# Performance work log

Hardware: AMD Instinct MI355X
Metric: run time of the kernel (lower is better)

Reference implementation:

```python
import jax, jax.numpy as jnp
import numpy as np

NEG_INF = -1e30

def setup_inputs() -> dict:
    key = jax.random.key(0)
    kC, kQ, kw = jax.random.split(key, 3)
    B, D, Lc, Lq = 32, 128, 2048, 64
    C = jax.random.normal(kC, (B, D, Lc), dtype=jnp.float32)
    Q = jax.random.normal(kQ, (B, D, Lq), dtype=jnp.float32)
    qmask = jnp.ones((B, Lq), dtype=jnp.float32)
    # trilinear weight, uniform(-sqrt(1/D), sqrt(1/D)) as in the torch init
    lim = (1.0 / D) ** 0.5
    w = jax.random.uniform(kw, (3 * D,), dtype=jnp.float32, minval=-lim, maxval=lim)
    return {"C": C, "Q": Q, "qmask": qmask, "w": w}

def reference(C, Q, qmask, w):
    # C: (B, D, Lc), Q: (B, D, Lq), qmask: (B, Lq), w: (3D,)
    Ct = jnp.transpose(C, (0, 2, 1))  # (B, Lc, D)
    Qt = jnp.transpose(Q, (0, 2, 1))  # (B, Lq, D)
    D = Ct.shape[-1]
    w1, w2, w3 = w[:D], w[D:2 * D], w[2 * D:]
    # trilinear similarity S[b,i,j] = Ct[b,i].w1 + Qt[b,j].w2 + (Ct[b,i]*Qt[b,j]).w3
    # computed WITHOUT the (B,Lc,Lq,3D) intermediate
    sc = Ct @ w1                                   # (B, Lc)
    sq = Qt @ w2                                   # (B, Lq)
    scq = jnp.einsum('bid,bjd->bij', Ct * w3, Qt)  # (B, Lc, Lq)
    S = sc[:, :, None] + sq[None if False else slice(None), None, :] + scq  # (B, Lc, Lq)
    m = qmask[:, None, :]                          # (B, 1, Lq)
    S1 = jax.nn.softmax(S * m + (1.0 - m) * NEG_INF, axis=2)  # over query axis
    S2 = jax.nn.softmax(S, axis=1)                             # over context axis
    A = jnp.einsum('bij,bjd->bid', S1, Qt)                     # (B, Lc, D)
    S1S2T = jnp.einsum('bij,bkj->bik', S1, S2)                 # (B, Lc, Lc) via S1 @ S2^T
    Bm = jnp.einsum('bik,bkd->bid', S1S2T, Ct)                 # (B, Lc, D)
    out = jnp.concatenate([Ct, A, Ct * A, Ct * Bm], axis=2)    # (B, Lc, 4D)
    # dropout is identity in eval mode
    return jnp.transpose(out, (0, 2, 1))                       # (B, 4D, Lc)
```

## Files before the change

kernel.cpp:

```cpp
#include <hip/hip_runtime.h>

#define LC 2048
#define DD 128
#define LQ 64
#define NPART 16
#define PAD 136

typedef unsigned short u16;
typedef unsigned int u32;
typedef __attribute__((ext_vector_type(8))) short bf16x8;
typedef __attribute__((ext_vector_type(4))) float f32x4;

__device__ inline u16 f2b(float f) {
  u32 u = __float_as_uint(f);
  u32 r = (u + 0x7fffu + ((u >> 16) & 1u)) >> 16;
  return (u16)r;
}
__device__ inline float b2f(u16 u) { return __uint_as_float(((u32)u) << 16); }
__device__ inline u32 pack2(float a, float b) {
  return (u32)f2b(a) | ((u32)f2b(b) << 16);
}

__global__ __launch_bounds__(256) void k13(const float* __restrict__ C,
                                           const float* __restrict__ Q,
                                           const float* __restrict__ w,
                                           const float* __restrict__ qmask,
                                           u16* __restrict__ S1g,
                                           float* __restrict__ Tu_part,
                                           float* __restrict__ Z_part, int B) {
  __shared__ u16 ldsA[128 * PAD];
  __shared__ u16 ldsB[64 * PAD];
  __shared__ float scL[128];
  __shared__ float sqs[64];
  __shared__ float mkS[64];
  int b = blockIdx.y, bx = blockIdx.x;
  int i0 = bx * 128, t = threadIdx.x;
  const float* Cb = C + (size_t)b * DD * LC;
  const float* Qb = Q + (size_t)b * DD * LQ;
  if (t < 64) mkS[t] = qmask[b * LQ + t];
  int i_st = t & 127, dh = t >> 7;
  float scp = 0.f;
  {
    const float* Cp = Cb + (size_t)dh * 64 * LC + i0 + i_st;
#pragma unroll
    for (int dp = 0; dp < 32; ++dp) {
      int d = dh * 64 + 2 * dp;
      float c0 = Cp[(size_t)(2 * dp) * LC];
      float c1 = Cp[(size_t)(2 * dp + 1) * LC];
      scp = fmaf(c0, w[d], fmaf(c1, w[d + 1], scp));
      *(u32*)&ldsA[i_st * PAD + d] = pack2(c0, c1);
    }
    if (dh == 0) scL[i_st] = scp;
  }
  {
    int j = t & 63, dg = t >> 6;
    const float* Qp = Qb + j;
    float sqp = 0.f;
#pragma unroll
    for (int dp = 0; dp < 16; ++dp) {
      int d = dg * 32 + 2 * dp;
      float q0 = Qp[(size_t)d * LQ];
      float q1 = Qp[(size_t)(d + 1) * LQ];
      sqp = fmaf(q0, w[DD + d], fmaf(q1, w[DD + d + 1], sqp));
      *(u32*)&ldsB[j * PAD + d] = pack2(q0 * w[2 * DD + d], q1 * w[2 * DD + d + 1]);
    }
    ((float*)&ldsB[j * PAD + 128])[dg] = sqp;
  }
  __syncthreads();
  if (dh == 1) scL[i_st] += scp;
  if (t < 64) {
    const float* pp = (const float*)&ldsB[t * PAD + 128];
    sqs[t] = pp[0] + pp[1] + pp[2] + pp[3];
  }
  int lane = t & 63, wv = t >> 6;
  int lr = lane & 15, kg = lane >> 4;
  f32x4 acc[2][4];
#pragma unroll
  for (int mt = 0; mt < 2; ++mt)
#pragma unroll
    for (int nt = 0; nt < 4; ++nt) acc[mt][nt] = (f32x4){0.f, 0.f, 0.f, 0.f};
#pragma unroll
  for (int ks = 0; ks < 4; ++ks) {
    bf16x8 af[2], bf[4];
#pragma unroll
    for (int mt = 0; mt < 2; ++mt)
      af[mt] = *(bf16x8*)&ldsA[((wv * 2 + mt) * 16 + lr) * PAD + ks * 32 + kg * 8];
#pragma unroll
    for (int nt = 0; nt < 4; ++nt)
      bf[nt] = *(bf16x8*)&ldsB[(nt * 16 + lr) * PAD + ks * 32 + kg * 8];
#pragma unroll
    for (int mt = 0; mt < 2; ++mt)
#pragma unroll
      for (int nt = 0; nt < 4; ++nt)
        acc[mt][nt] = __builtin_amdgcn_mfma_f32_16x16x32_bf16(af[mt], bf[nt],
                                                              acc[mt][nt], 0, 0, 0);
  }
  __syncthreads();
#pragma unroll
  for (int mt = 0; mt < 2; ++mt) {
    int ib = (wv * 2 + mt) * 16 + kg * 4;
    float ev[4][4];
    float ps[4] = {0.f, 0.f, 0.f, 0.f};
#pragma unroll
    for (int nt = 0; nt < 4; ++nt) {
      int j = nt * 16 + lr;
      float sqv = sqs[j];
      float mkv = mkS[j];
#pragma unroll
      for (int r = 0; r < 4; ++r) {
        float e = __expf(acc[mt][nt][r] + scL[ib + r] + sqv);
        ev[nt][r] = e;
        ps[r] = fmaf(mkv, e, ps[r]);
      }
    }
#pragma unroll
    for (int r = 0; r < 4; ++r) {
      ps[r] += __shfl_xor(ps[r], 1, 64);
      ps[r] += __shfl_xor(ps[r], 2, 64);
      ps[r] += __shfl_xor(ps[r], 4, 64);
      ps[r] += __shfl_xor(ps[r], 8, 64);
    }
#pragma unroll
    for (int nt = 0; nt < 4; ++nt) {
      int j = nt * 16 + lr;
      u32 pk[2] = {pack2(ev[nt][0], ev[nt][1]), pack2(ev[nt][2], ev[nt][3])};
      *(uint2*)&ldsB[j * PAD + ib] = *(uint2*)pk;
    }
    if (lr == 0) {
#pragma unroll
      for (int r = 0; r < 4; ++r) {
        int i = ib + r;
        ((float*)&ldsB[(i & 63) * PAD + 128])[i >> 6] = 1.f / fmaxf(ps[r], 1e-30f);
      }
    }
  }
  {
    int d = t >> 1, half = t & 1;
    const float* src = Cb + (size_t)d * LC + i0 + half * 64;
#pragma unroll
    for (int ip = 0; ip < 16; ++ip) {
      float4 v = *(const float4*)&src[ip * 4];
      u32 pk[2] = {pack2(v.x, v.y), pack2(v.z, v.w)};
      *(uint2*)&ldsA[d * PAD + half * 64 + ip * 4] = *(uint2*)pk;
    }
  }
  __syncthreads();
  if (t < 64) {
    const u32* row = (const u32*)&ldsB[t * PAD];
    float z = 0.f;
#pragma unroll
    for (int q = 0; q < 64; ++q) {
      u32 v = row[q];
      z += b2f((u16)v) + b2f((u16)(v >> 16));
    }
    Z_part[((size_t)bx * B + b) * LQ + t] = z;
  }
  {
    int i = t >> 1, half = t & 1;
    float inv = ((float*)&ldsB[(i & 63) * PAD + 128])[i >> 6];
    u32 opk[16];
#pragma unroll
    for (int q = 0; q < 16; ++q) {
      int j = half * 32 + 2 * q;
      float a0 = b2f(ldsB[j * PAD + i]) * mkS[j] * inv;
      float a1 = b2f(ldsB[(j + 1) * PAD + i]) * mkS[j + 1] * inv;
      opk[q] = pack2(a0, a1);
    }
    u16* dst = S1g + ((size_t)b * LC + i0 + i) * LQ + half * 32;
#pragma unroll
    for (int q = 0; q < 4; ++q) *(uint4*)&dst[q * 8] = *(uint4*)&opk[q * 4];
  }
  f32x4 tacc[2][4];
#pragma unroll
  for (int mt = 0; mt < 2; ++mt)
#pragma unroll
    for (int nt = 0; nt < 4; ++nt) tacc[mt][nt] = (f32x4){0.f, 0.f, 0.f, 0.f};
#pragma unroll
  for (int ks = 0; ks < 4; ++ks) {
    bf16x8 af[2], bf[4];
#pragma unroll
    for (int mt = 0; mt < 2; ++mt)
      af[mt] = *(bf16x8*)&ldsA[((wv * 2 + mt) * 16 + lr) * PAD + ks * 32 + kg * 8];
#pragma unroll
    for (int nt = 0; nt < 4; ++nt)
      bf[nt] = *(bf16x8*)&ldsB[(nt * 16 + lr) * PAD + ks * 32 + kg * 8];
#pragma unroll
    for (int mt = 0; mt < 2; ++mt)
#pragma unroll
      for (int nt = 0; nt < 4; ++nt)
        tacc[mt][nt] = __builtin_amdgcn_mfma_f32_16x16x32_bf16(af[mt], bf[nt],
                                                               tacc[mt][nt], 0, 0, 0);
  }
  float* Tp = Tu_part + ((size_t)bx * B + b) * LQ * DD;
#pragma unroll
  for (int mt = 0; mt < 2; ++mt)
#pragma unroll
    for (int nt = 0; nt < 4; ++nt) {
      int j = nt * 16 + lr;
      int db = (wv * 2 + mt) * 16 + kg * 4;
      *(f32x4*)&Tp[(size_t)j * DD + db] = tacc[mt][nt];
    }
}

__global__ __launch_bounds__(256) void k3b(const float* __restrict__ Tu_part,
                                           const float* __restrict__ Z_part,
                                           u16* __restrict__ TzT, int B) {
  __shared__ float Tsm[16][68];
  __shared__ float ziL[64];
  int b = blockIdx.y, d0 = blockIdx.x * 16;
  int t = threadIdx.x;
  int dd = t & 15, jg = t >> 4;
  float acc[4] = {};
#pragma unroll
  for (int p = 0; p < NPART; ++p) {
    const float* src = Tu_part + ((size_t)p * B + b) * LQ * DD + d0 + dd;
#pragma unroll
    for (int jj = 0; jj < 4; ++jj) acc[jj] += src[(jg * 4 + jj) * DD];
  }
  if (t < 64) {
    float z = 0.f;
#pragma unroll
    for (int p = 0; p < NPART; ++p) z += Z_part[((size_t)p * B + b) * LQ + t];
    ziL[t] = 1.f / z;
  }
  *(float4*)&Tsm[dd][jg * 4] = make_float4(acc[0], acc[1], acc[2], acc[3]);
  __syncthreads();
  if (t < 128) {
    int d = t >> 3, seg = t & 7;
    u32 pk[4];
#pragma unroll
    for (int q = 0; q < 4; ++q) {
      int j = seg * 8 + q * 2;
      pk[q] = pack2(Tsm[d][j] * ziL[j], Tsm[d][j + 1] * ziL[j + 1]);
    }
    *(uint4*)&TzT[((size_t)b * DD + d0 + d) * LQ + seg * 8] = *(uint4*)pk;
  }
}

__global__ __launch_bounds__(256) void k4(const u16* __restrict__ S1g,
                                          const float* __restrict__ Q,
                                          const u16* __restrict__ TzT,
                                          const float* __restrict__ C,
                                          float* __restrict__ out) {
  int b = blockIdx.y, i0 = blockIdx.x * 128, t = threadIdx.x;
  int lane = t & 63, wv = t >> 6;
  int lr = lane & 15, kg = lane >> 4;
  bf16x8 Bf[2][2];
#pragma unroll
  for (int it = 0; it < 2; ++it) {
    size_t ri = (size_t)b * LC + i0 + wv * 32 + it * 16 + lr;
#pragma unroll
    for (int ks = 0; ks < 2; ++ks)
      Bf[it][ks] = *(const bf16x8*)&S1g[ri * LQ + ks * 32 + kg * 8];
  }
  const float* Qb = Q + (size_t)b * DD * LQ;
  const u16* Tzb = TzT + (size_t)b * DD * LQ;
  const float* Cb = C + (size_t)b * DD * LC + i0;
  float* outb = out + (size_t)b * 4 * DD * LC + i0;
#pragma unroll
  for (int dt = 0; dt < 8; ++dt) {
    int da = dt * 16 + lr;
    bf16x8 QA[2], TA[2];
#pragma unroll
    for (int ks = 0; ks < 2; ++ks) {
      const float* qp = Qb + da * LQ + ks * 32 + kg * 8;
      float4 q0 = *(const float4*)qp;
      float4 q1 = *(const float4*)(qp + 4);
      u32 pk[4] = {pack2(q0.x, q0.y), pack2(q0.z, q0.w), pack2(q1.x, q1.y),
                   pack2(q1.z, q1.w)};
      QA[ks] = *(bf16x8*)pk;
      TA[ks] = *(const bf16x8*)&Tzb[da * LQ + ks * 32 + kg * 8];
    }
#pragma unroll
    for (int it = 0; it < 2; ++it) {
      f32x4 accA = {0.f, 0.f, 0.f, 0.f}, accB = {0.f, 0.f, 0.f, 0.f};
      accA = __builtin_amdgcn_mfma_f32_16x16x32_bf16(QA[0], Bf[it][0], accA, 0, 0, 0);
      accA = __builtin_amdgcn_mfma_f32_16x16x32_bf16(QA[1], Bf[it][1], accA, 0, 0, 0);
      accB = __builtin_amdgcn_mfma_f32_16x16x32_bf16(TA[0], Bf[it][0], accB, 0, 0, 0);
      accB = __builtin_amdgcn_mfma_f32_16x16x32_bf16(TA[1], Bf[it][1], accB, 0, 0, 0);
      int ii = wv * 32 + it * 16 + lr;
#pragma unroll
      for (int r = 0; r < 4; ++r) {
        int d = dt * 16 + kg * 4 + r;
        float c = Cb[(size_t)d * LC + ii];
        float a = accA[r], bm = accB[r];
        outb[(size_t)d * LC + ii] = c;
        outb[(size_t)(DD + d) * LC + ii] = a;
        outb[(size_t)(2 * DD + d) * LC + ii] = c * a;
        outb[(size_t)(3 * DD + d) * LC + ii] = c * bm;
      }
    }
  }
}

extern "C" void kernel_launch(void* const* d_in, const int* in_sizes, int n_in,
                              void* d_out, int out_size, void* d_ws, size_t ws_size,
                              hipStream_t stream) {
  const float* C = (const float*)d_in[0];
  const float* Q = (const float*)d_in[1];
  const float* qmask = (const float*)d_in[2];
  const float* w = (const float*)d_in[3];
  float* out = (float*)d_out;
  int B = in_sizes[2] / LQ;

  char* p = (char*)d_ws;
  u16* S1g = (u16*)p;           p += (size_t)B * LC * LQ * 2;
  u16* TzT = (u16*)p;           p += (size_t)B * DD * LQ * 2;
  float* Tu_part = (float*)p;   p += (size_t)NPART * B * LQ * DD * 4;
  float* Z_part = (float*)p;

  k13<<<dim3(NPART, B), 256, 0, stream>>>(C, Q, w, qmask, S1g, Tu_part, Z_part, B);
  k3b<<<dim3(DD / 16, B), 256, 0, stream>>>(Tu_part, Z_part, TzT, B);
  k4<<<dim3(LC / 128, B), 256, 0, stream>>>(S1g, Q, TzT, C, out);
}
```

Measured before the change: 71.58 us.

## Halve row tiles, pre-convert Q to bf16, vectorize k4 output stores

The context tile in k13 and k4 shrinks from 128 to 64 rows. This doubles the grid and the number of partial sums, with LDS buffers and reductions reorganized to match. k3b now also converts Q to bf16 once, so k4 no longer repacks Q in every block. k4 swaps its MFMA operand roles so each lane holds 4 consecutive context positions, which lets it read C and write all four output planes with float4 accesses. The trade-off is that k3b must now reduce twice as many Tu partials, and the grid gets more blocks with less work each.

```diff
diff --git a/kernel.cpp b/kernel.cpp
--- a/kernel.cpp
+++ b/kernel.cpp
@@ -3,8 +3,9 @@
 #define LC 2048
 #define DD 128
 #define LQ 64
-#define NPART 16
-#define PAD 136
+#define NPART 32
+#define PADA 136
+#define PADC 72
 
 typedef unsigned short u16;
 typedef unsigned int u32;
@@ -28,29 +29,28 @@
                                            u16* __restrict__ S1g,
                                            float* __restrict__ Tu_part,
                                            float* __restrict__ Z_part, int B) {
-  __shared__ u16 ldsA[128 * PAD];
-  __shared__ u16 ldsB[64 * PAD];
-  __shared__ float scL[128];
-  __shared__ float sqs[64];
-  __shared__ float mkS[64];
+  __shared__ u16 ldsA[128 * PADC];
+  __shared__ u16 ldsB[64 * PADA];
+  __shared__ float scp4[4][64], sqp4[4][64];
+  __shared__ float scL[64], sqs[64], mkS[64], invL[64];
   int b = blockIdx.y, bx = blockIdx.x;
-  int i0 = bx * 128, t = threadIdx.x;
+  int i0 = bx * 64, t = threadIdx.x;
   const float* Cb = C + (size_t)b * DD * LC;
   const float* Qb = Q + (size_t)b * DD * LQ;
   if (t < 64) mkS[t] = qmask[b * LQ + t];
-  int i_st = t & 127, dh = t >> 7;
-  float scp = 0.f;
-  {
-    const float* Cp = Cb + (size_t)dh * 64 * LC + i0 + i_st;
-#pragma unroll
-    for (int dp = 0; dp < 32; ++dp) {
-      int d = dh * 64 + 2 * dp;
-      float c0 = Cp[(size_t)(2 * dp) * LC];
-      float c1 = Cp[(size_t)(2 * dp + 1) * LC];
+  {
+    int i = t & 63, dg = t >> 6;
+    const float* Cp = Cb + i0 + i;
+    float scp = 0.f;
+#pragma unroll
+    for (int dp = 0; dp < 16; ++dp) {
+      int d = dg * 32 + 2 * dp;
+      float c0 = Cp[(size_t)d * LC];
+      float c1 = Cp[(size_t)(d + 1) * LC];
       scp = fmaf(c0, w[d], fmaf(c1, w[d + 1], scp));
-      *(u32*)&ldsA[i_st * PAD + d] = pack2(c0, c1);
-    }
-    if (dh == 0) scL[i_st] = scp;
+      *(u32*)&ldsA[i * PADA + d] = pack2(c0, c1);
+    }
+    scp4[dg][i] = scp;
   }
   {
     int j = t & 63, dg = t >> 6;
@@ -62,53 +62,44 @@
       float q0 = Qp[(size_t)d * LQ];
       float q1 = Qp[(size_t)(d + 1) * LQ];
       sqp = fmaf(q0, w[DD + d], fmaf(q1, w[DD + d + 1], sqp));
-      *(u32*)&ldsB[j * PAD + d] = pack2(q0 * w[2 * DD + d], q1 * w[2 * DD + d + 1]);
-    }
-    ((float*)&ldsB[j * PAD + 128])[dg] = sqp;
+      *(u32*)&ldsB[j * PADA + d] = pack2(q0 * w[2 * DD + d], q1 * w[2 * DD + d + 1]);
+    }
+    sqp4[dg][j] = sqp;
   }
   __syncthreads();
-  if (dh == 1) scL[i_st] += scp;
-  if (t < 64) {
-    const float* pp = (const float*)&ldsB[t * PAD + 128];
-    sqs[t] = pp[0] + pp[1] + pp[2] + pp[3];
+  if (t < 64) scL[t] = scp4[0][t] + scp4[1][t] + scp4[2][t] + scp4[3][t];
+  else if (t < 128) {
+    int j = t - 64;
+    sqs[j] = sqp4[0][j] + sqp4[1][j] + sqp4[2][j] + sqp4[3][j];
   }
   int lane = t & 63, wv = t >> 6;
   int lr = lane & 15, kg = lane >> 4;
-  f32x4 acc[2][4];
-#pragma unroll
-  for (int mt = 0; mt < 2; ++mt)
-#pragma unroll
-    for (int nt = 0; nt < 4; ++nt) acc[mt][nt] = (f32x4){0.f, 0.f, 0.f, 0.f};
+  f32x4 acc[4];
+#pragma unroll
+  for (int nt = 0; nt < 4; ++nt) acc[nt] = (f32x4){0.f, 0.f, 0.f, 0.f};
 #pragma unroll
   for (int ks = 0; ks < 4; ++ks) {
-    bf16x8 af[2], bf[4];
-#pragma unroll
-    for (int mt = 0; mt < 2; ++mt)
-      af[mt] = *(bf16x8*)&ldsA[((wv * 2 + mt) * 16 + lr) * PAD + ks * 32 + kg * 8];
+    bf16x8 af = *(bf16x8*)&ldsA[(wv * 16 + lr) * PADA + ks * 32 + kg * 8];
+    bf16x8 bf[4];
 #pragma unroll
     for (int nt = 0; nt < 4; ++nt)
-      bf[nt] = *(bf16x8*)&ldsB[(nt * 16 + lr) * PAD + ks * 32 + kg * 8];
-#pragma unroll
-    for (int mt = 0; mt < 2; ++mt)
-#pragma unroll
-      for (int nt = 0; nt < 4; ++nt)
-        acc[mt][nt] = __builtin_amdgcn_mfma_f32_16x16x32_bf16(af[mt], bf[nt],
-                                                              acc[mt][nt], 0, 0, 0);
+      bf[nt] = *(bf16x8*)&ldsB[(nt * 16 + lr) * PADA + ks * 32 + kg * 8];
+#pragma unroll
+    for (int nt = 0; nt < 4; ++nt)
+      acc[nt] = __builtin_amdgcn_mfma_f32_16x16x32_bf16(af, bf[nt], acc[nt], 0, 0, 0);
   }
   __syncthreads();
-#pragma unroll
-  for (int mt = 0; mt < 2; ++mt) {
-    int ib = (wv * 2 + mt) * 16 + kg * 4;
+  {
+    int ib = wv * 16 + kg * 4;
     float ev[4][4];
     float ps[4] = {0.f, 0.f, 0.f, 0.f};
 #pragma unroll
     for (int nt = 0; nt < 4; ++nt) {
       int j = nt * 16 + lr;
-      float sqv = sqs[j];
-      float mkv = mkS[j];
+      float sqv = sqs[j], mkv = mkS[j];
 #pragma unroll
       for (int r = 0; r < 4; ++r) {
-        float e = __expf(acc[mt][nt][r] + scL[ib + r] + sqv);
+        float e = __expf(acc[nt][r] + scL[ib + r] + sqv);
         ev[nt][r] = e;
         ps[r] = fmaf(mkv, e, ps[r]);
       }
@@ -124,51 +115,48 @@
     for (int nt = 0; nt < 4; ++nt) {
       int j = nt * 16 + lr;
       u32 pk[2] = {pack2(ev[nt][0], ev[nt][1]), pack2(ev[nt][2], ev[nt][3])};
-      *(uint2*)&ldsB[j * PAD + ib] = *(uint2*)pk;
+      *(uint2*)&ldsB[j * PADC + ib] = *(uint2*)pk;
     }
     if (lr == 0) {
 #pragma unroll
-      for (int r = 0; r < 4; ++r) {
-        int i = ib + r;
-        ((float*)&ldsB[(i & 63) * PAD + 128])[i >> 6] = 1.f / fmaxf(ps[r], 1e-30f);
-      }
+      for (int r = 0; r < 4; ++r) invL[ib + r] = 1.f / fmaxf(ps[r], 1e-30f);
     }
   }
   {
     int d = t >> 1, half = t & 1;
-    const float* src = Cb + (size_t)d * LC + i0 + half * 64;
-#pragma unroll
-    for (int ip = 0; ip < 16; ++ip) {
+    const float* src = Cb + (size_t)d * LC + i0 + half * 32;
+#pragma unroll
+    for (int ip = 0; ip < 8; ++ip) {
       float4 v = *(const float4*)&src[ip * 4];
       u32 pk[2] = {pack2(v.x, v.y), pack2(v.z, v.w)};
-      *(uint2*)&ldsA[d * PAD + half * 64 + ip * 4] = *(uint2*)pk;
+      *(uint2*)&ldsA[d * PADC + half * 32 + ip * 4] = *(uint2*)pk;
     }
   }
   __syncthreads();
   if (t < 64) {
-    const u32* row = (const u32*)&ldsB[t * PAD];
+    const u32* row = (const u32*)&ldsB[t * PADC];
     float z = 0.f;
 #pragma unroll
-    for (int q = 0; q < 64; ++q) {
+    for (int q = 0; q < 32; ++q) {
       u32 v = row[q];
       z += b2f((u16)v) + b2f((u16)(v >> 16));
     }
     Z_part[((size_t)bx * B + b) * LQ + t] = z;
   }
   {
-    int i = t >> 1, half = t & 1;
-    float inv = ((float*)&ldsB[(i & 63) * PAD + 128])[i >> 6];
-    u32 opk[16];
-#pragma unroll
-    for (int q = 0; q < 16; ++q) {
-      int j = half * 32 + 2 * q;
-      float a0 = b2f(ldsB[j * PAD + i]) * mkS[j] * inv;
-      float a1 = b2f(ldsB[(j + 1) * PAD + i]) * mkS[j + 1] * inv;
+    int i = t >> 2, q4 = t & 3;
+    float inv = invL[i];
+    u32 opk[8];
+#pragma unroll
+    for (int q = 0; q < 8; ++q) {
+      int j = q4 * 16 + 2 * q;
+      float a0 = b2f(ldsB[j * PADC + i]) * mkS[j] * inv;
+      float a1 = b2f(ldsB[(j + 1) * PADC + i]) * mkS[j + 1] * inv;
       opk[q] = pack2(a0, a1);
     }
-    u16* dst = S1g + ((size_t)b * LC + i0 + i) * LQ + half * 32;
-#pragma unroll
-    for (int q = 0; q < 4; ++q) *(uint4*)&dst[q * 8] = *(uint4*)&opk[q * 4];
+    u16* dst = S1g + ((size_t)b * LC + i0 + i) * LQ + q4 * 16;
+    *(uint4*)&dst[0] = *(uint4*)&opk[0];
+    *(uint4*)&dst[8] = *(uint4*)&opk[4];
   }
   f32x4 tacc[2][4];
 #pragma unroll
@@ -176,14 +164,14 @@
 #pragma unroll
     for (int nt = 0; nt < 4; ++nt) tacc[mt][nt] = (f32x4){0.f, 0.f, 0.f, 0.f};
 #pragma unroll
-  for (int ks = 0; ks < 4; ++ks) {
+  for (int ks = 0; ks < 2; ++ks) {
     bf16x8 af[2], bf[4];
 #pragma unroll
     for (int mt = 0; mt < 2; ++mt)
-      af[mt] = *(bf16x8*)&ldsA[((wv * 2 + mt) * 16 + lr) * PAD + ks * 32 + kg * 8];
+      af[mt] = *(bf16x8*)&ldsA[((wv * 2 + mt) * 16 + lr) * PADC + ks * 32 + kg * 8];
 #pragma unroll
     for (int nt = 0; nt < 4; ++nt)
-      bf[nt] = *(bf16x8*)&ldsB[(nt * 16 + lr) * PAD + ks * 32 + kg * 8];
+      bf[nt] = *(bf16x8*)&ldsB[(nt * 16 + lr) * PADC + ks * 32 + kg * 8];
 #pragma unroll
     for (int mt = 0; mt < 2; ++mt)
 #pragma unroll
@@ -204,11 +192,19 @@
 
 __global__ __launch_bounds__(256) void k3b(const float* __restrict__ Tu_part,
                                            const float* __restrict__ Z_part,
-                                           u16* __restrict__ TzT, int B) {
+                                           const float* __restrict__ Q,
+                                           u16* __restrict__ TzT,
+                                           u16* __restrict__ Qbf, int B) {
   __shared__ float Tsm[16][68];
   __shared__ float ziL[64];
   int b = blockIdx.y, d0 = blockIdx.x * 16;
   int t = threadIdx.x;
+  {
+    int dq = d0 + (t >> 4), jq = (t & 15) * 4;
+    const float* qp = Q + ((size_t)b * DD + dq) * LQ + jq;
+    u32 pk[2] = {pack2(qp[0], qp[1]), pack2(qp[2], qp[3])};
+    *(uint2*)&Qbf[((size_t)b * DD + dq) * LQ + jq] = *(uint2*)pk;
+  }
   int dd = t & 15, jg = t >> 4;
   float acc[4] = {};
 #pragma unroll
@@ -238,58 +234,48 @@
 }
 
 __global__ __launch_bounds__(256) void k4(const u16* __restrict__ S1g,
-                                          const float* __restrict__ Q,
+                                          const u16* __restrict__ Qbf,
                                           const u16* __restrict__ TzT,
                                           const float* __restrict__ C,
                                           float* __restrict__ out) {
-  int b = blockIdx.y, i0 = blockIdx.x * 128, t = threadIdx.x;
+  int b = blockIdx.y, i0 = blockIdx.x * 64, t = threadIdx.x;
   int lane = t & 63, wv = t >> 6;
   int lr = lane & 15, kg = lane >> 4;
-  bf16x8 Bf[2][2];
-#pragma unroll
-  for (int it = 0; it < 2; ++it) {
-    size_t ri = (size_t)b * LC + i0 + wv * 32 + it * 16 + lr;
-#pragma unroll
-    for (int ks = 0; ks < 2; ++ks)
-      Bf[it][ks] = *(const bf16x8*)&S1g[ri * LQ + ks * 32 + kg * 8];
-  }
-  const float* Qb = Q + (size_t)b * DD * LQ;
+  bf16x8 Af[2];
+  {
+    size_t ri = ((size_t)b * LC + i0 + wv * 16 + lr) * LQ;
+    Af[0] = *(const bf16x8*)&S1g[ri + kg * 8];
+    Af[1] = *(const bf16x8*)&S1g[ri + 32 + kg * 8];
+  }
+  const u16* Qb = Qbf + (size_t)b * DD * LQ;
   const u16* Tzb = TzT + (size_t)b * DD * LQ;
   const float* Cb = C + (size_t)b * DD * LC + i0;
   float* outb = out + (size_t)b * 4 * DD * LC + i0;
-#pragma unroll
-  for (int dt = 0; dt < 8; ++dt) {
-    int da = dt * 16 + lr;
-    bf16x8 QA[2], TA[2];
+  int irow = wv * 16 + kg * 4;
+#pragma unroll
+  for (int nt = 0; nt < 8; ++nt) {
+    int d = nt * 16 + lr;
+    bf16x8 QB[2], TB[2];
 #pragma unroll
     for (int ks = 0; ks < 2; ++ks) {
-      const float* qp = Qb + da * LQ + ks * 32 + kg * 8;
-      float4 q0 = *(const float4*)qp;
-      float4 q1 = *(const float4*)(qp + 4);
-      u32 pk[4] = {pack2(q0.x, q0.y), pack2(q0.z, q0.w), pack2(q1.x, q1.y),
-                   pack2(q1.z, q1.w)};
-      QA[ks] = *(bf16x8*)pk;
-      TA[ks] = *(const bf16x8*)&Tzb[da * LQ + ks * 32 + kg * 8];
-    }
-#pragma unroll
-    for (int it = 0; it < 2; ++it) {
-      f32x4 accA = {0.f, 0.f, 0.f, 0.f}, accB = {0.f, 0.f, 0.f, 0.f};
-      accA = __builtin_amdgcn_mfma_f32_16x16x32_bf16(QA[0], Bf[it][0], accA, 0, 0, 0);
-      accA = __builtin_amdgcn_mfma_f32_16x16x32_bf16(QA[1], Bf[it][1], accA, 0, 0, 0);
-      accB = __builtin_amdgcn_mfma_f32_16x16x32_bf16(TA[0], Bf[it][0], accB, 0, 0, 0);
-      accB = __builtin_amdgcn_mfma_f32_16x16x32_bf16(TA[1], Bf[it][1], accB, 0, 0, 0);
-      int ii = wv * 32 + it * 16 + lr;
-#pragma unroll
-      for (int r = 0; r < 4; ++r) {
-        int d = dt * 16 + kg * 4 + r;
-        float c = Cb[(size_t)d * LC + ii];
-        float a = accA[r], bm = accB[r];
-        outb[(size_t)d * LC + ii] = c;
-        outb[(size_t)(DD + d) * LC + ii] = a;
-        outb[(size_t)(2 * DD + d) * LC + ii] = c * a;
-        outb[(size_t)(3 * DD + d) * LC + ii] = c * bm;
-      }
-    }
+      QB[ks] = *(const bf16x8*)&Qb[(size_t)d * LQ + ks * 32 + kg * 8];
+      TB[ks] = *(const bf16x8*)&Tzb[(size_t)d * LQ + ks * 32 + kg * 8];
+    }
+    f32x4 accA = {0.f, 0.f, 0.f, 0.f}, accB = {0.f, 0.f, 0.f, 0.f};
+    accA = __builtin_amdgcn_mfma_f32_16x16x32_bf16(Af[0], QB[0], accA, 0, 0, 0);
+    accA = __builtin_amdgcn_mfma_f32_16x16x32_bf16(Af[1], QB[1], accA, 0, 0, 0);
+    accB = __builtin_amdgcn_mfma_f32_16x16x32_bf16(Af[0], TB[0], accB, 0, 0, 0);
+    accB = __builtin_amdgcn_mfma_f32_16x16x32_bf16(Af[1], TB[1], accB, 0, 0, 0);
+    float4 c4 = *(const float4*)&Cb[(size_t)d * LC + irow];
+    float4 oA = make_float4(accA[0], accA[1], accA[2], accA[3]);
+    float4 oCA = make_float4(c4.x * accA[0], c4.y * accA[1], c4.z * accA[2],
+                             c4.w * accA[3]);
+    float4 oCB = make_float4(c4.x * accB[0], c4.y * accB[1], c4.z * accB[2],
+                             c4.w * accB[3]);
+    *(float4*)&outb[(size_t)d * LC + irow] = c4;
+    *(float4*)&outb[(size_t)(DD + d) * LC + irow] = oA;
+    *(float4*)&outb[(size_t)(2 * DD + d) * LC + irow] = oCA;
+    *(float4*)&outb[(size_t)(3 * DD + d) * LC + irow] = oCB;
   }
 }
 
@@ -306,10 +292,11 @@
   char* p = (char*)d_ws;
   u16* S1g = (u16*)p;           p += (size_t)B * LC * LQ * 2;
   u16* TzT = (u16*)p;           p += (size_t)B * DD * LQ * 2;
+  u16* Qbf = (u16*)p;           p += (size_t)B * DD * LQ * 2;
   float* Tu_part = (float*)p;   p += (size_t)NPART * B * LQ * DD * 4;
   float* Z_part = (float*)p;
 
-  k13<<<dim3(NPART, B), 256, 0, stream>>>(C, Q, w, qmask, S1g, Tu_part, Z_part, B);
-  k3b<<<dim3(DD / 16, B), 256, 0, stream>>>(Tu_part, Z_part, TzT, B);
-  k4<<<dim3(LC / 128, B), 256, 0, stream>>>(S1g, Q, TzT, C, out);
-}
+  k13<<<dim3(LC / 64, B), 256, 0, stream>>>(C, Q, w, qmask, S1g, Tu_part, Z_part, B);
+  k3b<<<dim3(DD / 16, B), 256, 0, stream>>>(Tu_part, Z_part, Q, TzT, Qbf, B);
+  k4<<<dim3(LC / 64, B), 256, 0, stream>>>(S1g, Qbf, TzT, C, out);
+}
```

Result: slower. 77.70 us (+8.5%).

## Precompute bf16 Q in k3b and swap MFMA operands in k4 for vectorized stores

Applied to the files above, without the earlier changes.

k3b now also converts Q to bf16 once into a workspace buffer, so k4 no longer repacks fp32 Q in every block. In k4 the MFMA operands are swapped so each lane's accumulator holds four consecutive context positions. That allows float4 loads of C and float4 stores for all four output slabs, where before each element was a scalar access. k4 tiles are halved to 64 rows, doubling the grid. The k13 grid now uses LC/128 instead of NPART, which is the same count (16), so this is unchanged.

```diff
diff --git a/kernel.cpp b/kernel.cpp
--- a/kernel.cpp
+++ b/kernel.cpp
@@ -204,11 +204,19 @@
 
 __global__ __launch_bounds__(256) void k3b(const float* __restrict__ Tu_part,
                                            const float* __restrict__ Z_part,
-                                           u16* __restrict__ TzT, int B) {
+                                           const float* __restrict__ Q,
+                                           u16* __restrict__ TzT,
+                                           u16* __restrict__ Qbf, int B) {
   __shared__ float Tsm[16][68];
   __shared__ float ziL[64];
   int b = blockIdx.y, d0 = blockIdx.x * 16;
   int t = threadIdx.x;
+  {
+    int dq = d0 + (t >> 4), jq = (t & 15) * 4;
+    const float* qp = Q + ((size_t)b * DD + dq) * LQ + jq;
+    u32 pk[2] = {pack2(qp[0], qp[1]), pack2(qp[2], qp[3])};
+    *(uint2*)&Qbf[((size_t)b * DD + dq) * LQ + jq] = *(uint2*)pk;
+  }
   int dd = t & 15, jg = t >> 4;
   float acc[4] = {};
 #pragma unroll
@@ -238,58 +246,48 @@
 }
 
 __global__ __launch_bounds__(256) void k4(const u16* __restrict__ S1g,
-                                          const float* __restrict__ Q,
+                                          const u16* __restrict__ Qbf,
                                           const u16* __restrict__ TzT,
                                           const float* __restrict__ C,
                                           float* __restrict__ out) {
-  int b = blockIdx.y, i0 = blockIdx.x * 128, t = threadIdx.x;
+  int b = blockIdx.y, i0 = blockIdx.x * 64, t = threadIdx.x;
   int lane = t & 63, wv = t >> 6;
   int lr = lane & 15, kg = lane >> 4;
-  bf16x8 Bf[2][2];
-#pragma unroll
-  for (int it = 0; it < 2; ++it) {
-    size_t ri = (size_t)b * LC + i0 + wv * 32 + it * 16 + lr;
-#pragma unroll
-    for (int ks = 0; ks < 2; ++ks)
-      Bf[it][ks] = *(const bf16x8*)&S1g[ri * LQ + ks * 32 + kg * 8];
-  }
-  const float* Qb = Q + (size_t)b * DD * LQ;
+  bf16x8 Af[2];
+  {
+    size_t ri = ((size_t)b * LC + i0 + wv * 16 + lr) * LQ;
+    Af[0] = *(const bf16x8*)&S1g[ri + kg * 8];
+    Af[1] = *(const bf16x8*)&S1g[ri + 32 + kg * 8];
+  }
+  const u16* Qb = Qbf + (size_t)b * DD * LQ;
   const u16* Tzb = TzT + (size_t)b * DD * LQ;
   const float* Cb = C + (size_t)b * DD * LC + i0;
   float* outb = out + (size_t)b * 4 * DD * LC + i0;
-#pragma unroll
-  for (int dt = 0; dt < 8; ++dt) {
-    int da = dt * 16 + lr;
-    bf16x8 QA[2], TA[2];
+  int irow = wv * 16 + kg * 4;
+#pragma unroll
+  for (int nt = 0; nt < 8; ++nt) {
+    int d = nt * 16 + lr;
+    bf16x8 QB[2], TB[2];
 #pragma unroll
     for (int ks = 0; ks < 2; ++ks) {
-      const float* qp = Qb + da * LQ + ks * 32 + kg * 8;
-      float4 q0 = *(const float4*)qp;
-      float4 q1 = *(const float4*)(qp + 4);
-      u32 pk[4] = {pack2(q0.x, q0.y), pack2(q0.z, q0.w), pack2(q1.x, q1.y),
-                   pack2(q1.z, q1.w)};
-      QA[ks] = *(bf16x8*)pk;
-      TA[ks] = *(const bf16x8*)&Tzb[da * LQ + ks * 32 + kg * 8];
-    }
-#pragma unroll
-    for (int it = 0; it < 2; ++it) {
-      f32x4 accA = {0.f, 0.f, 0.f, 0.f}, accB = {0.f, 0.f, 0.f, 0.f};
-      accA = __builtin_amdgcn_mfma_f32_16x16x32_bf16(QA[0], Bf[it][0], accA, 0, 0, 0);
-      accA = __builtin_amdgcn_mfma_f32_16x16x32_bf16(QA[1], Bf[it][1], accA, 0, 0, 0);
-      accB = __builtin_amdgcn_mfma_f32_16x16x32_bf16(TA[0], Bf[it][0], accB, 0, 0, 0);
-      accB = __builtin_amdgcn_mfma_f32_16x16x32_bf16(TA[1], Bf[it][1], accB, 0, 0, 0);
-      int ii = wv * 32 + it * 16 + lr;
-#pragma unroll
-      for (int r = 0; r < 4; ++r) {
-        int d = dt * 16 + kg * 4 + r;
-        float c = Cb[(size_t)d * LC + ii];
-        float a = accA[r], bm = accB[r];
-        outb[(size_t)d * LC + ii] = c;
-        outb[(size_t)(DD + d) * LC + ii] = a;
-        outb[(size_t)(2 * DD + d) * LC + ii] = c * a;
-        outb[(size_t)(3 * DD + d) * LC + ii] = c * bm;
-      }
-    }
+      QB[ks] = *(const bf16x8*)&Qb[(size_t)d * LQ + ks * 32 + kg * 8];
+      TB[ks] = *(const bf16x8*)&Tzb[(size_t)d * LQ + ks * 32 + kg * 8];
+    }
+    f32x4 accA = {0.f, 0.f, 0.f, 0.f}, accB = {0.f, 0.f, 0.f, 0.f};
+    accA = __builtin_amdgcn_mfma_f32_16x16x32_bf16(Af[0], QB[0], accA, 0, 0, 0);
+    accA = __builtin_amdgcn_mfma_f32_16x16x32_bf16(Af[1], QB[1], accA, 0, 0, 0);
+    accB = __builtin_amdgcn_mfma_f32_16x16x32_bf16(Af[0], TB[0], accB, 0, 0, 0);
+    accB = __builtin_amdgcn_mfma_f32_16x16x32_bf16(Af[1], TB[1], accB, 0, 0, 0);
+    float4 c4 = *(const float4*)&Cb[(size_t)d * LC + irow];
+    float4 oA = make_float4(accA[0], accA[1], accA[2], accA[3]);
+    float4 oCA = make_float4(c4.x * accA[0], c4.y * accA[1], c4.z * accA[2],
+                             c4.w * accA[3]);
+    float4 oCB = make_float4(c4.x * accB[0], c4.y * accB[1], c4.z * accB[2],
+                             c4.w * accB[3]);
+    *(float4*)&outb[(size_t)d * LC + irow] = c4;
+    *(float4*)&outb[(size_t)(DD + d) * LC + irow] = oA;
+    *(float4*)&outb[(size_t)(2 * DD + d) * LC + irow] = oCA;
+    *(float4*)&outb[(size_t)(3 * DD + d) * LC + irow] = oCB;
   }
 }
 
@@ -306,10 +304,11 @@
   char* p = (char*)d_ws;
   u16* S1g = (u16*)p;           p += (size_t)B * LC * LQ * 2;
   u16* TzT = (u16*)p;           p += (size_t)B * DD * LQ * 2;
+  u16* Qbf = (u16*)p;           p += (size_t)B * DD * LQ * 2;
   float* Tu_part = (float*)p;   p += (size_t)NPART * B * LQ * DD * 4;
   float* Z_part = (float*)p;
 
-  k13<<<dim3(NPART, B), 256, 0, stream>>>(C, Q, w, qmask, S1g, Tu_part, Z_part, B);
-  k3b<<<dim3(DD / 16, B), 256, 0, stream>>>(Tu_part, Z_part, TzT, B);
-  k4<<<dim3(LC / 128, B), 256, 0, stream>>>(S1g, Q, TzT, C, out);
-}
+  k13<<<dim3(LC / 128, B), 256, 0, stream>>>(C, Q, w, qmask, S1g, Tu_part, Z_part, B);
+  k3b<<<dim3(DD / 16, B), 256, 0, stream>>>(Tu_part, Z_part, Q, TzT, Qbf, B);
+  k4<<<dim3(LC / 64, B), 256, 0, stream>>>(S1g, Qbf, TzT, C, out);
+}
```

Result: faster. 69.92 us (-2.3%).
